# Optimization experiments

Hardware: AMD Instinct MI355X
Metric: run time of the kernel (lower is better)

Reference implementation:

```python
import jax, jax.numpy as jnp
import numpy as np
from jax import lax

B, N = 16, 2048
S0, S1, K = 256, 128, 32
EPS = 1e-5


def bn_relu(x, gamma, beta, axes):
    # training-mode BatchNorm (batch statistics) + ReLU; channel is last dim
    mean = jnp.mean(x, axis=axes, keepdims=True)
    var = jnp.var(x, axis=axes, keepdims=True)
    return jax.nn.relu((x - mean) * lax.rsqrt(var + EPS) * gamma + beta)


def fps(coords, s):
    # farthest point sampling, deterministic start at index 0. coords [B,N,3]
    b, n, _ = coords.shape
    def body(carry, _):
        dist, far = carry
        centroid = jnp.take_along_axis(coords, far[:, None, None], axis=1)  # [B,1,3]
        d = jnp.sum((coords - centroid) ** 2, axis=-1)                      # [B,N]
        dist = jnp.minimum(dist, d)
        return (dist, jnp.argmax(dist, axis=-1).astype(jnp.int32)), far
    init = (jnp.full((b, n), 1e10, coords.dtype), jnp.zeros((b,), jnp.int32))
    _, idx = lax.scan(body, init, None, length=s)
    return jnp.transpose(idx)  # [B,s]


def gather_points(pts, idx):
    # pts [B,N,C], idx [B,...] int -> [B,...,C]
    flat = idx.reshape(idx.shape[0], -1)[..., None]  # [B,M,1]
    out = jnp.take_along_axis(pts, flat, axis=1)     # [B,M,C]
    return out.reshape(*idx.shape, pts.shape[-1])


def sample_and_knn_group(s, k, coords, features):
    # coords [B,N,3], features [B,N,C] -> new_xyz [B,s,3], agg [B,s,k,2C]
    fps_idx = fps(coords, s)
    new_xyz = gather_points(coords, fps_idx)      # [B,s,3]
    center = gather_points(features, fps_idx)     # [B,s,C]
    d2 = jnp.sum((new_xyz[:, :, None, :] - coords[:, None, :, :]) ** 2, axis=-1)  # [B,s,N]
    _, knn_idx = lax.top_k(-d2, k)                # k smallest distances
    grouped = gather_points(features, knn_idx)    # [B,s,k,C]
    agg = jnp.concatenate(
        [grouped - center[:, :, None, :],
         jnp.broadcast_to(center[:, :, None, :], grouped.shape)], axis=-1)
    return new_xyz, agg


def sg_block(coords, features, s, k, w, gamma, beta):
    # conv1x1 -> BN -> ReLU -> max over k neighbors
    new_xyz, nf = sample_and_knn_group(s, k, coords, features)  # nf [B,s,k,d]
    h = jnp.einsum('bskd,od->bsko', nf, w)
    h = bn_relu(h, gamma, beta, axes=(0, 1, 2))
    return new_xyz, jnp.max(h, axis=2)  # [B,s,out]


def setup_inputs() -> dict:
    key = jax.random.key(0)
    ks = jax.random.split(key, 5)
    return {
        'x': jax.random.normal(ks[0], (B, 3, N), jnp.float32),
        'w1': jax.random.normal(ks[1], (64, 3), jnp.float32) * (1.0 / np.sqrt(3)),
        'g1': jnp.ones((64,), jnp.float32), 'b1': jnp.zeros((64,), jnp.float32),
        'w2': jax.random.normal(ks[2], (64, 64), jnp.float32) * 0.125,
        'g2': jnp.ones((64,), jnp.float32), 'b2': jnp.zeros((64,), jnp.float32),
        'w_sg0': jax.random.normal(ks[3], (128, 128), jnp.float32) * (1.0 / np.sqrt(128)),
        'g_sg0': jnp.ones((128,), jnp.float32), 'b_sg0': jnp.zeros((128,), jnp.float32),
        'w_sg1': jax.random.normal(ks[4], (256, 256), jnp.float32) * (1.0 / np.sqrt(256)),
        'g_sg1': jnp.ones((256,), jnp.float32), 'b_sg1': jnp.zeros((256,), jnp.float32),
    }


def reference(x, w1, g1, b1, w2, g2, b2, w_sg0, g_sg0, b_sg0, w_sg1, g_sg1, b_sg1):
    coords = jnp.transpose(x, (0, 2, 1))                   # [B,N,3]
    f = bn_relu(jnp.einsum('bnc,oc->bno', coords, w1), g1, b1, axes=(0, 1))  # [B,N,64]
    f = bn_relu(jnp.einsum('bnc,oc->bno', f, w2), g2, b2, axes=(0, 1))       # [B,N,64]
    xyz1, f1 = sg_block(coords, f, S0, K, w_sg0, g_sg0, b_sg0)   # [B,S0,128]
    _, f2 = sg_block(xyz1, f1, S1, K, w_sg1, g_sg1, b_sg1)       # [B,S1,256]
    return jnp.transpose(f2, (0, 2, 1))                           # [B,256,S1]
```

## Files before the change

### kernel.cpp

```cpp
#include <hip/hip_runtime.h>
#include <float.h>

#define BATCH 16
#define NPTS  2048
#define NS0   256
#define NS1   128
#define KK    32
#define EPSV  1e-5f
#define MROWS 32768.0f
#define M0F   131072.0f
#define M1F   65536.0f

__device__ __forceinline__ float sqdist(float ax,float ay,float az,float bx,float by,float bz){
  float dx=__fsub_rn(ax,bx), dy=__fsub_rn(ay,by), dz=__fsub_rn(az,bz);
  return __fadd_rn(__fadd_rn(__fmul_rn(dx,dx),__fmul_rn(dy,dy)),__fmul_rn(dz,dz));
}

template<int CTRL,int RM>
__device__ __forceinline__ float dpp_fmax_s(float x){
  int t = __builtin_amdgcn_update_dpp((int)0xFF800000, __float_as_int(x), CTRL, RM, 0xf, false);
  return fmaxf(x, __int_as_float(t));
}
template<int CTRL,int RM>
__device__ __forceinline__ unsigned dpp_umin_s(unsigned x){
  unsigned t = (unsigned)__builtin_amdgcn_update_dpp(-1, (int)x, CTRL, RM, 0xf, false);
  return t<x ? t : x;
}
__device__ __forceinline__ void wave_argmax_f32(float v, unsigned idx, float& mall, int& sel){
  float m=v;
  m=dpp_fmax_s<0x111,0xf>(m); m=dpp_fmax_s<0x112,0xf>(m); m=dpp_fmax_s<0x114,0xf>(m);
  m=dpp_fmax_s<0x118,0xf>(m); m=dpp_fmax_s<0x142,0xa>(m); m=dpp_fmax_s<0x143,0xc>(m);
  mall = __int_as_float(__builtin_amdgcn_readlane(__float_as_int(m),63));
  unsigned c = (v==mall)? idx : 0xFFFFFFFFu;
  c=dpp_umin_s<0x111,0xf>(c); c=dpp_umin_s<0x112,0xf>(c); c=dpp_umin_s<0x114,0xf>(c);
  c=dpp_umin_s<0x118,0xf>(c); c=dpp_umin_s<0x142,0xa>(c); c=dpp_umin_s<0x143,0xc>(c);
  sel = (int)(unsigned)__builtin_amdgcn_readlane((int)c,63);
}

template<int CTRL,int RM>
__device__ __forceinline__ unsigned long long dpp_umin64_s(unsigned long long x){
  unsigned tlo=(unsigned)__builtin_amdgcn_update_dpp(-1,(int)(unsigned)x,        CTRL,RM,0xf,false);
  unsigned thi=(unsigned)__builtin_amdgcn_update_dpp(-1,(int)(unsigned)(x>>32), CTRL,RM,0xf,false);
  unsigned long long t=((unsigned long long)thi<<32)|tlo;
  return t<x ? t : x;
}
__device__ __forceinline__ int wave_argmin_f32(float v, unsigned idx){
  unsigned long long k = ((unsigned long long)__float_as_uint(v)<<32) | (unsigned long long)idx;
  k=dpp_umin64_s<0x111,0xf>(k); k=dpp_umin64_s<0x112,0xf>(k); k=dpp_umin64_s<0x114,0xf>(k);
  k=dpp_umin64_s<0x118,0xf>(k); k=dpp_umin64_s<0x142,0xa>(k); k=dpp_umin64_s<0x143,0xc>(k);
  return (int)(unsigned)__builtin_amdgcn_readlane((int)(unsigned)k,63);
}


__device__ void embed1_body(int bid, const float* __restrict__ x, const float* __restrict__ w1,
                            float* __restrict__ coords, float* __restrict__ t1,
                            float* __restrict__ accS, float* __restrict__ accQ){
  __shared__ float w[192];
  __shared__ float xs[3][64];
  __shared__ float fin[64][65];
  __shared__ float ls[64], lq[64];
  int tid = threadIdx.x;
  if (tid < 192) w[tid] = w1[tid];
  int base = bid*64;
  int b = base / NPTS, n0 = base % NPTS;
  if (tid < 192){
    int ch = tid>>6, i = tid&63;
    xs[ch][i] = x[((size_t)b*3+ch)*NPTS + n0 + i];
  } else {
    int t = tid - 192;
    ls[t]=0.f; lq[t]=0.f;
  }
  __syncthreads();
  if (tid < 64){
    coords[(size_t)(base+tid)*3+0]=xs[0][tid];
    coords[(size_t)(base+tid)*3+1]=xs[1][tid];
    coords[(size_t)(base+tid)*3+2]=xs[2][tid];
  }
  int p = tid>>2, c0 = (tid&3)<<4;
  float cx=xs[0][p], cy=xs[1][p], cz=xs[2][p];
  #pragma unroll
  for(int j=0;j<16;j++){
    int c = c0+j;
    fin[p][c] = cx*w[c*3+0] + cy*w[c*3+1] + cz*w[c*3+2];
  }
  __syncthreads();
  float s_=0.f, q_=0.f;
  for(int i=tid;i<4096;i+=256){
    int pp=i>>6, c=i&63;
    float v = fin[pp][c];
    t1[(size_t)base*64 + i] = v;
    s_+=v; q_+=v*v;
  }
  atomicAdd(&ls[tid&63], s_);
  atomicAdd(&lq[tid&63], q_);
  __syncthreads();
  if(tid<64){ atomicAdd(accS+tid, ls[tid]); atomicAdd(accQ+tid, lq[tid]); }
}

__device__ void wt_body(int gid, const float* __restrict__ w0, float* __restrict__ wt0,
                        const float* __restrict__ w1, float* __restrict__ wt1){
  if(gid < 128*128){
    int o = gid % 128, c = gid / 128;
    wt0[gid] = w0[o*128 + c];
  } else {
    int g2 = gid - 128*128;
    if(g2 >= 256*256) return;
    int o = g2 % 256, c = g2 / 256;
    wt1[g2] = w1[o*256 + c];
  }
}

__device__ void embed2_body(int bid, const float* __restrict__ t1, const float* __restrict__ w2,
                            const float* __restrict__ accS, const float* __restrict__ accQ,
                            const float* __restrict__ g1, const float* __restrict__ b1,
                            float* __restrict__ t2,
                            float* __restrict__ acc2S, float* __restrict__ acc2Q,
                            float* ls, float* lq, char* smem){
  float (*fin)[64] = (float(*)[64])smem;
  float* sm = (float*)smem + 4096;
  float* sr = sm+64; float* sg = sr+64; float* sb = sg+64;
  int tid = threadIdx.x;
  if (tid<64){
    float S=accS[tid], Q=accQ[tid];
    float m = S/MROWS, v = Q/MROWS - m*m; if(v<0.f) v=0.f;
    sm[tid]=m; sr[tid]=rsqrtf(v+EPSV); sg[tid]=g1[tid]; sb[tid]=b1[tid];
    ls[tid]=0.f; lq[tid]=0.f;
  }
  __syncthreads();
  int base = bid*64;
  for(int i=tid;i<4096;i+=256){
    int p=i>>6, c=i&63;
    float v = t1[(size_t)(base+p)*64 + c];
    v = (v - sm[c])*sr[c]*sg[c] + sb[c];
    fin[p][c] = v>0.f ? v : 0.f;
  }
  __syncthreads();
  int o = tid & 63, p0 = tid>>6;
  float acc[16];
  #pragma unroll
  for(int i=0;i<16;i++) acc[i]=0.f;
  for(int cc=0; cc<64; cc+=4){
    float4 wv = *(const float4*)(w2 + o*64 + cc);
    #pragma unroll
    for(int i=0;i<16;i++){
      float4 f4 = *(const float4*)&fin[p0 + i*4][cc];
      acc[i] += f4.x*wv.x + f4.y*wv.y + f4.z*wv.z + f4.w*wv.w;
    }
  }
  float s=0.f,q=0.f;
  #pragma unroll
  for(int i=0;i<16;i++){
    float v = acc[i];
    t2[(size_t)(base+p0+i*4)*64 + o] = v;
    s+=v; q+=v*v;
  }
  atomicAdd(&ls[o], s);
  atomicAdd(&lq[o], q);
  __syncthreads();
  if(tid<64){ atomicAdd(acc2S+tid, ls[tid]); atomicAdd(acc2Q+tid, lq[tid]); }
}

template<int P, int S, int T>
__device__ void fps_body(int b, const float* __restrict__ x, int* __restrict__ outIdx,
                         float* __restrict__ outXyz, char* smem){
  constexpr int PPT = P/T;
  constexpr int NW  = T/64;
  float* sx=(float*)smem; float* sy=sx+P; float* sz=sy+P;
  int* sidx=(int*)(sz+P);
  unsigned long long* rv64=(unsigned long long*)(sidx+S);
  int tid = threadIdx.x;
  const float* xb = x + (size_t)b*3*P;
  float px[PPT], py[PPT], pz[PPT], dist[PPT];
  #pragma unroll
  for(int i=0;i<PPT;i++){
    int n = i*T + tid;
    float X=xb[n], Y=xb[P+n], Z=xb[2*P+n];
    px[i]=X; py[i]=Y; pz[i]=Z; dist[i]=1e10f;
    sx[n]=X; sy[n]=Y; sz[n]=Z;
  }
  __syncthreads();
  int cur = 0;
  float cx=sx[0], cy=sy[0], cz=sz[0];
  for(int s=0;s<S;s++){
    if(tid==0) sidx[s]=cur;
    if(s==S-1) break;
    float bv=-FLT_MAX; int bi=0;
    #pragma unroll
    for(int i=0;i<PPT;i++){
      float d = sqdist(px[i],py[i],pz[i],cx,cy,cz);
      float nd = fminf(dist[i], d);
      dist[i]=nd;
      int n = i*T + tid;
      if(nd>bv){ bv=nd; bi=n; }
    }
    float mall; int sel;
    wave_argmax_f32(bv,(unsigned)bi,mall,sel);
    int sl = s & 1;
    if((tid&63)==0) rv64[sl*NW+(tid>>6)] = ((unsigned long long)__float_as_uint(mall)<<32)|(unsigned)(~sel);
    __syncthreads();
    unsigned long long wk = rv64[sl*NW];
    #pragma unroll
    for(int w=1;w<NW;w++){ unsigned long long t = rv64[sl*NW+w]; if(t>wk) wk=t; }
    cur = (int)(~(unsigned)wk);
    cx=sx[cur]; cy=sy[cur]; cz=sz[cur];
  }
  __syncthreads();
  for(int i=tid; i<S; i+=T){
    int id = sidx[i];
    outIdx[b*S+i] = id;
    outXyz[((size_t)b*S+i)*3+0] = sx[id];
    outXyz[((size_t)b*S+i)*3+1] = sy[id];
    outXyz[((size_t)b*S+i)*3+2] = sz[id];
  }
}

template<int P, int S>
__device__ void fps_wave_body(int b, const float* __restrict__ pts, int* __restrict__ outIdx,
                              float* __restrict__ outXyz, char* smem){
  constexpr int PPT = P/64;
  float4* sp = (float4*)smem;
  int* sidx = (int*)(smem + P*sizeof(float4));
  int lane = threadIdx.x;
  const float* p = pts + (size_t)b*P*3;
  float px[PPT], py[PPT], pz[PPT], dist[PPT];
  #pragma unroll
  for(int i=0;i<PPT;i++){
    int n = i*64 + lane;
    float X=p[n*3], Y=p[n*3+1], Z=p[n*3+2];
    px[i]=X; py[i]=Y; pz[i]=Z; dist[i]=1e10f;
    sp[n] = make_float4(X,Y,Z,0.f);
  }
  __syncthreads();
  int cur = 0;
  float cx=sp[0].x, cy=sp[0].y, cz=sp[0].z;
  for(int s=0;s<S;s++){
    if(lane==0) sidx[s]=cur;
    if(s==S-1) break;
    float bv=-FLT_MAX; int bi=0;
    #pragma unroll
    for(int i=0;i<PPT;i++){
      float d = sqdist(px[i],py[i],pz[i],cx,cy,cz);
      float nd = fminf(dist[i], d);
      dist[i]=nd;
      int n = i*64 + lane;
      if(nd>bv){ bv=nd; bi=n; }
    }
    float mall; int sel;
    wave_argmax_f32(bv,(unsigned)bi,mall,sel);
    cur = sel;
    float4 cp = sp[cur];
    cx=cp.x; cy=cp.y; cz=cp.z;
  }
  __syncthreads();
  for(int i=lane; i<S; i+=64){
    int id = sidx[i];
    float4 cp = sp[id];
    outIdx[b*S+i] = id;
    outXyz[((size_t)b*S+i)*3+0] = cp.x;
    outXyz[((size_t)b*S+i)*3+1] = cp.y;
    outXyz[((size_t)b*S+i)*3+2] = cp.z;
  }
}

template<int P>
__device__ void knn_compute(const float* __restrict__ p, float qx, float qy, float qz,
                            int* outRow){
  constexpr int E = P/64;
  int lane = threadIdx.x & 63;
  float dl[E];
  float b1=FLT_MAX, b2=FLT_MAX;
  unsigned i1=0xFFFFFFFFu, i2=0xFFFFFFFFu, consumed=0u;
  #pragma unroll
  for(int i=0;i<E;i++){
    unsigned n = i*64 + lane;
    float v = sqdist(qx,qy,qz,p[n*3],p[n*3+1],p[n*3+2]);
    dl[i] = v;
    bool lt1 = v<b1, lt2 = v<b2;
    float    nb2 = lt1 ? b1 : (lt2 ? v : b2);
    unsigned ni2 = lt1 ? i1 : (lt2 ? n : i2);
    b1 = lt1 ? v : b1; i1 = lt1 ? n : i1;
    b2 = nb2; i2 = ni2;
  }
  for(int j=0;j<KK;j++){
    int sel = wave_argmin_f32(b1, i1);
    if(lane==0) outRow[j] = sel;
    if((sel & 63) == lane){
      consumed |= 1u << (sel >> 6);
      b1 = b2; i1 = i2;
      b2 = FLT_MAX; i2 = 0xFFFFFFFFu;
      if(b1 == FLT_MAX){
        #pragma unroll
        for(int i=0;i<E;i++){
          float v = ((consumed>>i)&1u) ? FLT_MAX : dl[i];
          unsigned n = i*64 + lane;
          bool lt1 = v<b1, lt2 = v<b2;
          float    nb2 = lt1 ? b1 : (lt2 ? v : b2);
          unsigned ni2 = lt1 ? i1 : (lt2 ? n : i2);
          b1 = lt1 ? v : b1; i1 = lt1 ? n : i1;
          b2 = nb2; i2 = ni2;
        }
      }
    }
  }
}

template<int C, int P, int MODE>
__device__ void pass1_body(int bq, const float* __restrict__ feats, const float* __restrict__ feats2,
                           const int* knnrow, int ci, const float* __restrict__ WT,
                           float* __restrict__ hmax, float* __restrict__ hmin,
                           float* __restrict__ part, int S,
                           const float* __restrict__ accS, const float* __restrict__ accQ,
                           const float* __restrict__ bg, const float* __restrict__ bb,
                           char* smem){
  constexpr int O   = 2*C;
  constexpr int TPB = C;
  constexpr int C4  = C/4;
  constexpr int OG  = O/8;
  constexpr int LDC = C+4;
  float* gfp = (float*)smem;
  float* cf  = gfp + KK*LDC;
  float* sa  = cf + C;
  float* sbb = sa + C;
  float* sct = sbb + C;
  int tid = threadIdx.x;
  int b = bq / S;
  const float* fb = feats + (size_t)b*P*C;
  const float* fb2 = (MODE==2) ? feats2 + (size_t)b*P*C : nullptr;
  {
    float Mv = (MODE==1) ? MROWS : M0F;
    float S_=accS[tid], Q_=accQ[tid];
    float m = S_/Mv, vv = Q_/Mv - m*m; if(vv<0.f) vv=0.f;
    float a = rsqrtf(vv+EPSV)*bg[tid];
    float sh = bb[tid] - m*a;
    sa[tid]=a; sbb[tid]=sh;
    float raw;
    if(MODE==1) raw = fb[(size_t)ci*C + tid];
    else        raw = (a>=0.f) ? fb[(size_t)ci*C + tid] : fb2[(size_t)ci*C + tid];
    float cv = a*raw + sh;
    cf[tid] = cv>0.f ? cv : 0.f;
  }
  __syncthreads();
  for(int i=tid; i<KK*C4; i+=TPB){
    int k = i/C4, d4 = i - k*C4;
    size_t row = (size_t)knnrow[k]*C;
    float4 a4 = *(const float4*)&sa[d4*4];
    float4 s4 = *(const float4*)&sbb[d4*4];
    float4 c4 = *(const float4*)&cf[d4*4];
    float4 g  = ((const float4*)(fb + row))[d4];
    float4 r;
    if(MODE==2){
      float4 g2 = ((const float4*)(fb2 + row))[d4];
      float gx = (a4.x>=0.f? g.x : g2.x)*a4.x + s4.x; gx = gx>0.f?gx:0.f;
      float gy = (a4.y>=0.f? g.y : g2.y)*a4.y + s4.y; gy = gy>0.f?gy:0.f;
      float gz = (a4.z>=0.f? g.z : g2.z)*a4.z + s4.z; gz = gz>0.f?gz:0.f;
      float gw = (a4.w>=0.f? g.w : g2.w)*a4.w + s4.w; gw = gw>0.f?gw:0.f;
      r.x=gx-c4.x; r.y=gy-c4.y; r.z=gz-c4.z; r.w=gw-c4.w;
    } else {
      float gx = a4.x*g.x+s4.x; gx = gx>0.f?gx:0.f;
      float gy = a4.y*g.y+s4.y; gy = gy>0.f?gy:0.f;
      float gz = a4.z*g.z+s4.z; gz = gz>0.f?gz:0.f;
      float gw = a4.w*g.w+s4.w; gw = gw>0.f?gw:0.f;
      r.x=gx-c4.x; r.y=gy-c4.y; r.z=gz-c4.z; r.w=gw-c4.w;
    }
    *(float4*)&gfp[k*LDC + d4*4] = r;
  }
  __syncthreads();
  {
    int o2 = tid*2;
    float ct0=0.f, ct1=0.f;
    for(int c=0;c<C;c+=4){
      float4 c4 = *(const float4*)&cf[c];
      #pragma unroll
      for(int t=0;t<4;t++){
        float cv = ((const float*)&c4)[t];
        float2 wh = *(const float2*)&WT[(size_t)(C+c+t)*O + o2];
        ct0 += cv*wh.x; ct1 += cv*wh.y;
      }
    }
    sct[o2]=ct0; sct[o2+1]=ct1;
  }
  __syncthreads();
  int kg = tid / OG;
  int og = tid % OG;
  float acc[8][8];
  #pragma unroll
  for(int a=0;a<8;a++)
    #pragma unroll
    for(int bb2=0;bb2<8;bb2++) acc[a][bb2]=0.f;
  for(int dc=0; dc<C4; dc++){
    float4 g4[8];
    #pragma unroll
    for(int jk=0;jk<8;jk++) g4[jk] = *(const float4*)&gfp[(kg*8+jk)*LDC + dc*4];
    #pragma unroll
    for(int t=0;t<4;t++){
      const float* wrow = WT + (size_t)(dc*4+t)*O + og*8;
      float4 wa = *(const float4*)wrow;
      float4 wb = *(const float4*)(wrow+4);
      #pragma unroll
      for(int jk=0;jk<8;jk++){
        float gs = ((const float*)&g4[jk])[t];
        acc[jk][0] += gs*wa.x; acc[jk][1] += gs*wa.y; acc[jk][2] += gs*wa.z; acc[jk][3] += gs*wa.w;
        acc[jk][4] += gs*wb.x; acc[jk][5] += gs*wb.y; acc[jk][6] += gs*wb.z; acc[jk][7] += gs*wb.w;
      }
    }
  }
  float tmx[8],tmn[8],tsm[8],tsq[8];
  #pragma unroll
  for(int jo=0;jo<8;jo++){
    int o = og*8+jo;
    float ct = sct[o];
    float s=0.f,q=0.f,mx=-FLT_MAX,mn=FLT_MAX;
    #pragma unroll
    for(int jk=0;jk<8;jk++){
      float h = acc[jk][jo] + ct;
      s+=h; q+=h*h; mx=fmaxf(mx,h); mn=fminf(mn,h);
    }
    tmx[jo]=mx; tmn[jo]=mn; tsm[jo]=s; tsq[jo]=q;
  }
  if constexpr (TPB==64){
    #pragma unroll
    for(int jo=0;jo<8;jo++){
      tmx[jo]=fmaxf(tmx[jo],__shfl_xor(tmx[jo],16)); tmx[jo]=fmaxf(tmx[jo],__shfl_xor(tmx[jo],32));
      tmn[jo]=fminf(tmn[jo],__shfl_xor(tmn[jo],16)); tmn[jo]=fminf(tmn[jo],__shfl_xor(tmn[jo],32));
      tsm[jo]+=__shfl_xor(tsm[jo],16); tsm[jo]+=__shfl_xor(tsm[jo],32);
      tsq[jo]+=__shfl_xor(tsq[jo],16); tsq[jo]+=__shfl_xor(tsq[jo],32);
    }
    if(tid<OG){
      #pragma unroll
      for(int jo=0;jo<8;jo++){
        int o = tid*8+jo;
        hmax[(size_t)bq*O+o]=tmx[jo]; hmin[(size_t)bq*O+o]=tmn[jo];
        part[(size_t)bq*2*O+o]=tsm[jo]; part[(size_t)bq*2*O+O+o]=tsq[jo];
      }
    }
  } else {
    #pragma unroll
    for(int jo=0;jo<8;jo++){
      tmx[jo]=fmaxf(tmx[jo],__shfl_xor(tmx[jo],32));
      tmn[jo]=fminf(tmn[jo],__shfl_xor(tmn[jo],32));
      tsm[jo]+=__shfl_xor(tsm[jo],32);
      tsq[jo]+=__shfl_xor(tsq[jo],32);
    }
    int wv = tid>>6;
    if((tid&63)<32){
      int og_ = tid&31;
      size_t rb = (size_t)bq*2 + wv;
      #pragma unroll
      for(int jo=0;jo<8;jo++){
        int o = og_*8+jo;
        hmax[rb*O+o]=tmx[jo]; hmin[rb*O+o]=tmn[jo];
        part[rb*2*O+o]=tsm[jo]; part[rb*2*O+O+o]=tsq[jo];
      }
    }
  }
}


__global__ __launch_bounds__(256) void k_embed1_wt(const float* __restrict__ x, const float* __restrict__ w1,
                         float* __restrict__ coords, float* __restrict__ t1,
                         const float* __restrict__ wsg0, float* __restrict__ wt0,
                         const float* __restrict__ wsg1, float* __restrict__ wt1,
                         float* __restrict__ acc1S, float* __restrict__ acc1Q){
  if(blockIdx.x < 512) embed1_body(blockIdx.x, x, w1, coords, t1, acc1S, acc1Q);
  else wt_body((blockIdx.x-512)*256 + threadIdx.x, wsg0, wt0, wsg1, wt1);
}

__global__ __launch_bounds__(256, 1) void k_fps0_embed2(const float* __restrict__ x,
                         int* __restrict__ fps0, float* __restrict__ xyz0,
                         const float* __restrict__ t1, const float* __restrict__ w2,
                         const float* __restrict__ acc1S, const float* __restrict__ acc1Q,
                         const float* __restrict__ g1, const float* __restrict__ b1,
                         float* __restrict__ t2,
                         float* __restrict__ acc2S, float* __restrict__ acc2Q){
  extern __shared__ char smem[];
  __shared__ float ls[64], lq[64];
  if(blockIdx.x < BATCH) fps_body<NPTS,NS0,256>(blockIdx.x, x, fps0, xyz0, smem);
  else embed2_body(blockIdx.x-BATCH, t1, w2, acc1S, acc1Q, g1, b1, t2, acc2S, acc2Q, ls, lq, smem);
}

__global__ __launch_bounds__(64, 2) void k_fps1_p1a(const float* __restrict__ xyz0,
                         int* __restrict__ fps1, float* __restrict__ xyz1,
                         const float* __restrict__ coords, const float* __restrict__ t2,
                         const int* __restrict__ fps0, const float* __restrict__ wt0,
                         float* __restrict__ hmax0, float* __restrict__ hmin0, float* __restrict__ part0,
                         const float* __restrict__ acc2S, const float* __restrict__ acc2Q,
                         const float* __restrict__ g2, const float* __restrict__ b2){
  __shared__ __align__(16) char SU[10112];
  if(blockIdx.x < BATCH){
    fps_wave_body<NS0,NS1>(blockIdx.x, xyz0, fps1, xyz1, SU);
    return;
  }
  int bq = blockIdx.x - BATCH;
  int b = bq / NS0;
  int* sknn = (int*)(SU + 9984);
  const float* pc = coords + (size_t)b*NPTS*3;
  float qx=xyz0[(size_t)bq*3], qy=xyz0[(size_t)bq*3+1], qz=xyz0[(size_t)bq*3+2];
  knn_compute<NPTS>(pc, qx, qy, qz, sknn);
  __syncthreads();
  pass1_body<64,NPTS,1>(bq, t2, nullptr, sknn, fps0[bq], wt0, hmax0, hmin0, part0, NS0,
                        acc2S, acc2Q, g2, b2, SU);
}

__global__ __launch_bounds__(256) void k_statsB(const float* __restrict__ part, int W,
                                                float* __restrict__ acc){
  int tid = threadIdx.x;
  int r0 = blockIdx.x*64;
  for(int c=tid; c<W; c+=256){
    float a=0.f;
    for(int r=0;r<64;r++) a += part[(size_t)(r0+r)*W + c];
    atomicAdd(acc+c, a);
  }
}

__global__ __launch_bounds__(128, 2) void k_knn1_p1b(const float* __restrict__ xyz0,
                         const float* __restrict__ xyz1, const int* __restrict__ fps1,
                         const float* __restrict__ hmax0, const float* __restrict__ hmin0,
                         const float* __restrict__ wt1,
                         float* __restrict__ hmax1, float* __restrict__ hmin1, float* __restrict__ part1,
                         const float* __restrict__ accB0S, const float* __restrict__ accB0Q,
                         const float* __restrict__ gsg0, const float* __restrict__ bsg0){
  __shared__ __align__(16) char SU[19584];
  int bq = blockIdx.x;
  int b = bq / NS1;
  int* sknn = (int*)(SU + 19456);
  if(threadIdx.x < 64){
    const float* pts = xyz0 + (size_t)b*NS0*3;
    float qx=xyz1[(size_t)bq*3], qy=xyz1[(size_t)bq*3+1], qz=xyz1[(size_t)bq*3+2];
    knn_compute<NS0>(pts, qx, qy, qz, sknn);
  }
  __syncthreads();
  pass1_body<128,NS0,2>(bq, hmax0, hmin0, sknn, fps1[bq], wt1, hmax1, hmin1, part1, NS1,
                        accB0S, accB0Q, gsg0, bsg0, SU);
}

__global__ __launch_bounds__(256) void k_post1tr(const float* __restrict__ hmax, const float* __restrict__ hmin,
        const float* __restrict__ aS, const float* __restrict__ aQ,
        const float* __restrict__ g, const float* __restrict__ bb, float* __restrict__ out){
  __shared__ float ssc[64], ssh[64];
  __shared__ float tile[64][129];
  int tid = threadIdx.x;
  int blk = blockIdx.x; int b = blk>>2; int c0 = (blk&3)*64;
  if(tid<64){
    int o = c0+tid;
    float m = aS[o]/M1F, v = aQ[o]/M1F - m*m; if(v<0.f) v=0.f;
    float sc = rsqrtf(v+EPSV)*g[o];
    ssc[tid]=sc; ssh[tid]=bb[o]-m*sc;
  }
  __syncthreads();
  for(int i=tid; i<128*64; i+=256){
    int r=i>>6, ch=i&63;
    size_t rb = (size_t)(b*NS1+r)*2;
    float sc = ssc[ch];
    float va = hmax[rb*256 + c0+ch], vb = hmax[(rb+1)*256 + c0+ch];
    float wa = hmin[rb*256 + c0+ch], wb = hmin[(rb+1)*256 + c0+ch];
    float h = (sc>=0.f) ? fmaxf(va,vb) : fminf(wa,wb);
    float v = h*sc + ssh[ch];
    tile[ch][r] = v>0.f ? v : 0.f;
  }
  __syncthreads();
  for(int i=tid; i<64*128; i+=256){
    int ch=i>>7, s=i&127;
    out[(size_t)b*(256*NS1) + (size_t)(c0+ch)*NS1 + s] = tile[ch][s];
  }
}

extern "C" void kernel_launch(void* const* d_in, const int* in_sizes, int n_in,
                              void* d_out, int out_size, void* d_ws, size_t ws_size,
                              hipStream_t stream){
  const float* x    = (const float*)d_in[0];
  const float* w1   = (const float*)d_in[1];
  const float* g1   = (const float*)d_in[2];
  const float* b1   = (const float*)d_in[3];
  const float* w2   = (const float*)d_in[4];
  const float* g2   = (const float*)d_in[5];
  const float* b2   = (const float*)d_in[6];
  const float* wsg0 = (const float*)d_in[7];
  const float* gsg0 = (const float*)d_in[8];
  const float* bsg0 = (const float*)d_in[9];
  const float* wsg1 = (const float*)d_in[10];
  const float* gsg1 = (const float*)d_in[11];
  const float* bsg1 = (const float*)d_in[12];
  float* out = (float*)d_out;

  float* wsf = (float*)d_ws;
  float* coords = wsf;                    wsf += BATCH*NPTS*3;
  float* t1     = wsf;                    wsf += BATCH*NPTS*64;
  float* t2     = wsf;                    wsf += BATCH*NPTS*64;
  float* acc1S=wsf; wsf+=64;  float* acc1Q=wsf; wsf+=64;
  float* acc2S=wsf; wsf+=64;  float* acc2Q=wsf; wsf+=64;
  float* accB0=wsf; wsf+=256;
  float* accB1=wsf; wsf+=512;
  int*   fps0 = (int*)wsf;                wsf += BATCH*NS0;
  float* xyz0 = wsf;                      wsf += BATCH*NS0*3;
  float* hmax0= wsf;                      wsf += BATCH*NS0*128;
  float* hmin0= wsf;                      wsf += BATCH*NS0*128;
  float* part0= wsf;                      wsf += BATCH*NS0*2*128;
  int*   fps1 = (int*)wsf;                wsf += BATCH*NS1;
  float* xyz1 = wsf;                      wsf += BATCH*NS1*3;
  float* wt0  = wsf;                      wsf += 128*128;
  float* wt1  = wsf;                      wsf += 256*256;
  float* part1 = t1;
  float* hmax1 = t2;
  float* hmin1 = t2 + BATCH*NS1*2*256;

  const int DYN_L3 = (NPTS*3 + NS0)*4 + 2*4*8;

  hipMemsetAsync(acc1S, 0, 1024*sizeof(float), stream);
  k_embed1_wt<<<dim3(832), dim3(256), 0, stream>>>(x, w1, coords, t1, wsg0, wt0, wsg1, wt1,
                                                   acc1S, acc1Q);
  k_fps0_embed2<<<dim3(BATCH+512), dim3(256), DYN_L3, stream>>>(x, fps0, xyz0,
                                                  t1, w2, acc1S, acc1Q, g1, b1, t2, acc2S, acc2Q);
  k_fps1_p1a<<<dim3(BATCH + BATCH*NS0), dim3(64), 0, stream>>>(xyz0, fps1, xyz1,
                                                  coords, t2, fps0, wt0,
                                                  hmax0, hmin0, part0,
                                                  acc2S, acc2Q, g2, b2);
  k_statsB<<<dim3(64), dim3(256), 0, stream>>>(part0, 256, accB0);
  k_knn1_p1b<<<dim3(BATCH*NS1), dim3(128), 0, stream>>>(xyz0, xyz1, fps1,
                                                  hmax0, hmin0, wt1,
                                                  hmax1, hmin1, part1,
                                                  accB0, accB0+128, gsg0, bsg0);
  k_statsB<<<dim3(64), dim3(256), 0, stream>>>(part1, 512, accB1);
  k_post1tr<<<dim3(64), dim3(256), 0, stream>>>(hmax1, hmin1, accB1, accB1+256, gsg1, bsg1, out);
}
```

Measured before the change: 394.2 us.

## Stream FPS0 progress into persistent mega-kernel overlapping KNN/pass1a and FPS1

Splits FPS0 out of the embed2 kernel and merges FPS0, FPS1 and the first KNN+conv pass into one persistent kernel that takes work tickets from an atomic counter. FPS0 publishes its sampled indices and coordinates incrementally, raising a per-batch progress flag every 32 samples. KNN/pass1a waves spin-wait on that flag, so neighbour search for early centroids can start while FPS is still running. The change also packs four single-wave work items into each 256-thread block. It adds spin-wait and memory-ordering risk and depends on ticket order to avoid deadlock.

```diff
diff --git a/kernel.cpp b/kernel.cpp
--- a/kernel.cpp
+++ b/kernel.cpp
@@ -49,6 +49,19 @@
   k=dpp_umin64_s<0x111,0xf>(k); k=dpp_umin64_s<0x112,0xf>(k); k=dpp_umin64_s<0x114,0xf>(k);
   k=dpp_umin64_s<0x118,0xf>(k); k=dpp_umin64_s<0x142,0xa>(k); k=dpp_umin64_s<0x143,0xc>(k);
   return (int)(unsigned)__builtin_amdgcn_readlane((int)(unsigned)k,63);
+}
+
+__device__ __forceinline__ void wave_sync(){
+  asm volatile("s_waitcnt lgkmcnt(0)" ::: "memory");
+  __builtin_amdgcn_sched_barrier(0);
+}
+
+__device__ __forceinline__ void wait_ge(int* flag, int want){
+  for(int t=0; t<(1<<20); ++t){
+    if(__hip_atomic_load(flag, __ATOMIC_RELAXED, __HIP_MEMORY_SCOPE_AGENT) >= want) break;
+    __builtin_amdgcn_s_sleep(2);
+  }
+  asm volatile("" ::: "memory");
 }
 
 
@@ -162,7 +175,7 @@
 
 template<int P, int S, int T>
 __device__ void fps_body(int b, const float* __restrict__ x, int* __restrict__ outIdx,
-                         float* __restrict__ outXyz, char* smem){
+                         float* __restrict__ outXyz, char* smem, int* prog){
   constexpr int PPT = P/T;
   constexpr int NW  = T/64;
   float* sx=(float*)smem; float* sy=sx+P; float* sz=sy+P;
@@ -182,7 +195,14 @@
   int cur = 0;
   float cx=sx[0], cy=sy[0], cz=sz[0];
   for(int s=0;s<S;s++){
-    if(tid==0) sidx[s]=cur;
+    if(tid==0){
+      sidx[s]=cur;
+      size_t o = (size_t)b*S + s;
+      outIdx[o]=cur;
+      outXyz[o*3+0]=cx; outXyz[o*3+1]=cy; outXyz[o*3+2]=cz;
+      if((s&31)==31)
+        __hip_atomic_store(prog+b, s+1, __ATOMIC_RELEASE, __HIP_MEMORY_SCOPE_AGENT);
+    }
     if(s==S-1) break;
     float bv=-FLT_MAX; int bi=0;
     #pragma unroll
@@ -212,25 +232,30 @@
     outXyz[((size_t)b*S+i)*3+1] = sy[id];
     outXyz[((size_t)b*S+i)*3+2] = sz[id];
   }
+  __syncthreads();
+  if(tid==0)
+    __hip_atomic_store(prog+b, S, __ATOMIC_RELEASE, __HIP_MEMORY_SCOPE_AGENT);
 }
 
 template<int P, int S>
-__device__ void fps_wave_body(int b, const float* __restrict__ pts, int* __restrict__ outIdx,
-                              float* __restrict__ outXyz, char* smem){
+__device__ void fps1_wave(int b, float* __restrict__ pts, int* __restrict__ outIdx,
+                          float* __restrict__ outXyz, char* smem){
   constexpr int PPT = P/64;
   float4* sp = (float4*)smem;
   int* sidx = (int*)(smem + P*sizeof(float4));
-  int lane = threadIdx.x;
-  const float* p = pts + (size_t)b*P*3;
+  int lane = threadIdx.x & 63;
+  float* p = pts + (size_t)b*P*3;
   float px[PPT], py[PPT], pz[PPT], dist[PPT];
   #pragma unroll
   for(int i=0;i<PPT;i++){
     int n = i*64 + lane;
-    float X=p[n*3], Y=p[n*3+1], Z=p[n*3+2];
+    float X=__hip_atomic_load(p+n*3+0, __ATOMIC_RELAXED, __HIP_MEMORY_SCOPE_AGENT);
+    float Y=__hip_atomic_load(p+n*3+1, __ATOMIC_RELAXED, __HIP_MEMORY_SCOPE_AGENT);
+    float Z=__hip_atomic_load(p+n*3+2, __ATOMIC_RELAXED, __HIP_MEMORY_SCOPE_AGENT);
     px[i]=X; py[i]=Y; pz[i]=Z; dist[i]=1e10f;
     sp[n] = make_float4(X,Y,Z,0.f);
   }
-  __syncthreads();
+  wave_sync();
   int cur = 0;
   float cx=sp[0].x, cy=sp[0].y, cz=sp[0].z;
   for(int s=0;s<S;s++){
@@ -251,7 +276,7 @@
     float4 cp = sp[cur];
     cx=cp.x; cy=cp.y; cz=cp.z;
   }
-  __syncthreads();
+  wave_sync();
   for(int i=lane; i<S; i+=64){
     int id = sidx[i];
     float4 cp = sp[id];
@@ -300,6 +325,117 @@
           b2 = nb2; i2 = ni2;
         }
       }
+    }
+  }
+}
+
+__device__ void pass1a_wave(int bq, const float* __restrict__ feats,
+                            const int* knnrow, int ci, const float* __restrict__ WT,
+                            float* __restrict__ hmax, float* __restrict__ hmin,
+                            float* __restrict__ part,
+                            const float* __restrict__ accS, const float* __restrict__ accQ,
+                            const float* __restrict__ bg, const float* __restrict__ bb,
+                            char* smem){
+  constexpr int C=64, O=128, C4=16, OG=16, LDC=68;
+  float* gfp = (float*)smem;
+  float* cf  = gfp + KK*LDC;
+  float* sa  = cf + C;
+  float* sbb = sa + C;
+  float* sct = sbb + C;
+  int lane = threadIdx.x & 63;
+  int b = bq >> 8;
+  const float* fb = feats + (size_t)b*NPTS*C;
+  {
+    float S_=accS[lane], Q_=accQ[lane];
+    float m = S_/MROWS, vv = Q_/MROWS - m*m; if(vv<0.f) vv=0.f;
+    float a = rsqrtf(vv+EPSV)*bg[lane];
+    float sh = bb[lane] - m*a;
+    sa[lane]=a; sbb[lane]=sh;
+    float raw = fb[(size_t)ci*C + lane];
+    float cv = a*raw + sh;
+    cf[lane] = cv>0.f ? cv : 0.f;
+  }
+  wave_sync();
+  for(int i=lane; i<KK*C4; i+=64){
+    int k = i>>4, d4 = i&15;
+    size_t row = (size_t)knnrow[k]*C;
+    float4 a4 = *(const float4*)&sa[d4*4];
+    float4 s4 = *(const float4*)&sbb[d4*4];
+    float4 c4 = *(const float4*)&cf[d4*4];
+    float4 g  = ((const float4*)(fb + row))[d4];
+    float gx = a4.x*g.x+s4.x; gx = gx>0.f?gx:0.f;
+    float gy = a4.y*g.y+s4.y; gy = gy>0.f?gy:0.f;
+    float gz = a4.z*g.z+s4.z; gz = gz>0.f?gz:0.f;
+    float gw = a4.w*g.w+s4.w; gw = gw>0.f?gw:0.f;
+    float4 r; r.x=gx-c4.x; r.y=gy-c4.y; r.z=gz-c4.z; r.w=gw-c4.w;
+    *(float4*)&gfp[k*LDC + d4*4] = r;
+  }
+  wave_sync();
+  {
+    int o2 = lane*2;
+    float ct0=0.f, ct1=0.f;
+    for(int c=0;c<C;c+=4){
+      float4 c4 = *(const float4*)&cf[c];
+      #pragma unroll
+      for(int t=0;t<4;t++){
+        float cv = ((const float*)&c4)[t];
+        float2 wh = *(const float2*)&WT[(size_t)(C+c+t)*O + o2];
+        ct0 += cv*wh.x; ct1 += cv*wh.y;
+      }
+    }
+    sct[o2]=ct0; sct[o2+1]=ct1;
+  }
+  wave_sync();
+  int kg = lane >> 4;
+  int og = lane & 15;
+  float acc[8][8];
+  #pragma unroll
+  for(int a=0;a<8;a++)
+    #pragma unroll
+    for(int bb2=0;bb2<8;bb2++) acc[a][bb2]=0.f;
+  for(int dc=0; dc<C4; dc++){
+    float4 g4[8];
+    #pragma unroll
+    for(int jk=0;jk<8;jk++) g4[jk] = *(const float4*)&gfp[(kg*8+jk)*LDC + dc*4];
+    #pragma unroll
+    for(int t=0;t<4;t++){
+      const float* wrow = WT + (size_t)(dc*4+t)*O + og*8;
+      float4 wa = *(const float4*)wrow;
+      float4 wb = *(const float4*)(wrow+4);
+      #pragma unroll
+      for(int jk=0;jk<8;jk++){
+        float gs = ((const float*)&g4[jk])[t];
+        acc[jk][0] += gs*wa.x; acc[jk][1] += gs*wa.y; acc[jk][2] += gs*wa.z; acc[jk][3] += gs*wa.w;
+        acc[jk][4] += gs*wb.x; acc[jk][5] += gs*wb.y; acc[jk][6] += gs*wb.z; acc[jk][7] += gs*wb.w;
+      }
+    }
+  }
+  float tmx[8],tmn[8],tsm[8],tsq[8];
+  #pragma unroll
+  for(int jo=0;jo<8;jo++){
+    int o = og*8+jo;
+    float ct = sct[o];
+    float s=0.f,q=0.f,mx=-FLT_MAX,mn=FLT_MAX;
+    #pragma unroll
+    for(int jk=0;jk<8;jk++){
+      float h = acc[jk][jo] + ct;
+      s+=h; q+=h*h; mx=fmaxf(mx,h); mn=fminf(mn,h);
+    }
+    tmx[jo]=mx; tmn[jo]=mn; tsm[jo]=s; tsq[jo]=q;
+  }
+  #pragma unroll
+  for(int jo=0;jo<8;jo++){
+    tmx[jo]=fmaxf(tmx[jo],__shfl_xor(tmx[jo],16)); tmx[jo]=fmaxf(tmx[jo],__shfl_xor(tmx[jo],32));
+    tmn[jo]=fminf(tmn[jo],__shfl_xor(tmn[jo],16)); tmn[jo]=fminf(tmn[jo],__shfl_xor(tmn[jo],32));
+    tsm[jo]+=__shfl_xor(tsm[jo],16); tsm[jo]+=__shfl_xor(tsm[jo],32);
+    tsq[jo]+=__shfl_xor(tsq[jo],16); tsq[jo]+=__shfl_xor(tsq[jo],32);
+  }
+  if(lane<OG){
+    #pragma unroll
+    for(int jo=0;jo<8;jo++){
+      int o = lane*8+jo;
+      hmax[(size_t)bq*O+o]=tmx[jo]; hmin[(size_t)bq*O+o]=tmn[jo];
+      part[(size_t)bq*2*O+o]=tsm[jo]; part[(size_t)bq*2*O+O+o]=tsq[jo];
     }
   }
 }
@@ -417,40 +553,22 @@
     }
     tmx[jo]=mx; tmn[jo]=mn; tsm[jo]=s; tsq[jo]=q;
   }
-  if constexpr (TPB==64){
+  #pragma unroll
+  for(int jo=0;jo<8;jo++){
+    tmx[jo]=fmaxf(tmx[jo],__shfl_xor(tmx[jo],32));
+    tmn[jo]=fminf(tmn[jo],__shfl_xor(tmn[jo],32));
+    tsm[jo]+=__shfl_xor(tsm[jo],32);
+    tsq[jo]+=__shfl_xor(tsq[jo],32);
+  }
+  int wv = tid>>6;
+  if((tid&63)<32){
+    int og_ = tid&31;
+    size_t rb = (size_t)bq*2 + wv;
     #pragma unroll
     for(int jo=0;jo<8;jo++){
-      tmx[jo]=fmaxf(tmx[jo],__shfl_xor(tmx[jo],16)); tmx[jo]=fmaxf(tmx[jo],__shfl_xor(tmx[jo],32));
-      tmn[jo]=fminf(tmn[jo],__shfl_xor(tmn[jo],16)); tmn[jo]=fminf(tmn[jo],__shfl_xor(tmn[jo],32));
-      tsm[jo]+=__shfl_xor(tsm[jo],16); tsm[jo]+=__shfl_xor(tsm[jo],32);
-      tsq[jo]+=__shfl_xor(tsq[jo],16); tsq[jo]+=__shfl_xor(tsq[jo],32);
-    }
-    if(tid<OG){
-      #pragma unroll
-      for(int jo=0;jo<8;jo++){
-        int o = tid*8+jo;
-        hmax[(size_t)bq*O+o]=tmx[jo]; hmin[(size_t)bq*O+o]=tmn[jo];
-        part[(size_t)bq*2*O+o]=tsm[jo]; part[(size_t)bq*2*O+O+o]=tsq[jo];
-      }
-    }
-  } else {
-    #pragma unroll
-    for(int jo=0;jo<8;jo++){
-      tmx[jo]=fmaxf(tmx[jo],__shfl_xor(tmx[jo],32));
-      tmn[jo]=fminf(tmn[jo],__shfl_xor(tmn[jo],32));
-      tsm[jo]+=__shfl_xor(tsm[jo],32);
-      tsq[jo]+=__shfl_xor(tsq[jo],32);
-    }
-    int wv = tid>>6;
-    if((tid&63)<32){
-      int og_ = tid&31;
-      size_t rb = (size_t)bq*2 + wv;
-      #pragma unroll
-      for(int jo=0;jo<8;jo++){
-        int o = og_*8+jo;
-        hmax[rb*O+o]=tmx[jo]; hmin[rb*O+o]=tmn[jo];
-        part[rb*2*O+o]=tsm[jo]; part[rb*2*O+O+o]=tsq[jo];
-      }
+      int o = og_*8+jo;
+      hmax[rb*O+o]=tmx[jo]; hmin[rb*O+o]=tmn[jo];
+      part[rb*2*O+o]=tsm[jo]; part[rb*2*O+O+o]=tsq[jo];
     }
   }
 }
@@ -465,40 +583,62 @@
   else wt_body((blockIdx.x-512)*256 + threadIdx.x, wsg0, wt0, wsg1, wt1);
 }
 
-__global__ __launch_bounds__(256, 1) void k_fps0_embed2(const float* __restrict__ x,
-                         int* __restrict__ fps0, float* __restrict__ xyz0,
-                         const float* __restrict__ t1, const float* __restrict__ w2,
+__global__ __launch_bounds__(256, 1) void k_embed2(const float* __restrict__ t1, const float* __restrict__ w2,
                          const float* __restrict__ acc1S, const float* __restrict__ acc1Q,
                          const float* __restrict__ g1, const float* __restrict__ b1,
                          float* __restrict__ t2,
                          float* __restrict__ acc2S, float* __restrict__ acc2Q){
   extern __shared__ char smem[];
   __shared__ float ls[64], lq[64];
-  if(blockIdx.x < BATCH) fps_body<NPTS,NS0,256>(blockIdx.x, x, fps0, xyz0, smem);
-  else embed2_body(blockIdx.x-BATCH, t1, w2, acc1S, acc1Q, g1, b1, t2, acc2S, acc2Q, ls, lq, smem);
-}
-
-__global__ __launch_bounds__(64, 2) void k_fps1_p1a(const float* __restrict__ xyz0,
-                         int* __restrict__ fps1, float* __restrict__ xyz1,
-                         const float* __restrict__ coords, const float* __restrict__ t2,
-                         const int* __restrict__ fps0, const float* __restrict__ wt0,
+  embed2_body(blockIdx.x, t1, w2, acc1S, acc1Q, g1, b1, t2, acc2S, acc2Q, ls, lq, smem);
+}
+
+#define NT_FPS0  16
+#define NT_FPS1E 20
+#define NT_ALL   1044
+__global__ __launch_bounds__(256) void k_mega(const float* __restrict__ x,
+                         int* __restrict__ fps0i, float* __restrict__ xyz0,
+                         const float* __restrict__ t2,
+                         const float* __restrict__ acc2S, const float* __restrict__ acc2Q,
+                         const float* __restrict__ coords, const float* __restrict__ wt0,
                          float* __restrict__ hmax0, float* __restrict__ hmin0, float* __restrict__ part0,
-                         const float* __restrict__ acc2S, const float* __restrict__ acc2Q,
-                         const float* __restrict__ g2, const float* __restrict__ b2){
-  __shared__ __align__(16) char SU[10112];
-  if(blockIdx.x < BATCH){
-    fps_wave_body<NS0,NS1>(blockIdx.x, xyz0, fps1, xyz1, SU);
-    return;
-  }
-  int bq = blockIdx.x - BATCH;
-  int b = bq / NS0;
-  int* sknn = (int*)(SU + 9984);
-  const float* pc = coords + (size_t)b*NPTS*3;
-  float qx=xyz0[(size_t)bq*3], qy=xyz0[(size_t)bq*3+1], qz=xyz0[(size_t)bq*3+2];
-  knn_compute<NPTS>(pc, qx, qy, qz, sknn);
-  __syncthreads();
-  pass1_body<64,NPTS,1>(bq, t2, nullptr, sknn, fps0[bq], wt0, hmax0, hmin0, part0, NS0,
-                        acc2S, acc2Q, g2, b2, SU);
+                         const float* __restrict__ g2, const float* __restrict__ b2,
+                         int* __restrict__ fps1i, float* __restrict__ xyz1,
+                         int* prog, int* tck){
+  extern __shared__ __align__(16) char SU[];
+  __shared__ int sTk;
+  int tid = threadIdx.x;
+  for(;;){
+    if(tid==0) sTk = atomicAdd(tck, 1);
+    __syncthreads();
+    int tk = sTk;
+    __syncthreads();
+    if(tk >= NT_ALL) return;
+    if(tk < NT_FPS0){
+      fps_body<NPTS,NS0,256>(tk, x, fps0i, xyz0, SU, prog);
+    } else if(tk < NT_FPS1E){
+      int wv = tid>>6;
+      int b4 = (tk-NT_FPS0)*4 + wv;
+      wait_ge(prog + b4, NS0);
+      fps1_wave<NS0,NS1>(b4, xyz0, fps1i, xyz1, SU + wv*4608);
+    } else {
+      int q = tk - NT_FPS1E;
+      int wv = tid>>6;
+      int b = q & 15;
+      int s = ((q>>4)<<2) + wv;
+      int bq = (b<<8) + s;
+      char* W = SU + wv*10112;
+      int* sknn = (int*)(W + 9984);
+      wait_ge(prog + b, s + 1);
+      float qx = __hip_atomic_load(xyz0+(size_t)bq*3+0, __ATOMIC_RELAXED, __HIP_MEMORY_SCOPE_AGENT);
+      float qy = __hip_atomic_load(xyz0+(size_t)bq*3+1, __ATOMIC_RELAXED, __HIP_MEMORY_SCOPE_AGENT);
+      float qz = __hip_atomic_load(xyz0+(size_t)bq*3+2, __ATOMIC_RELAXED, __HIP_MEMORY_SCOPE_AGENT);
+      int   ci = __hip_atomic_load(fps0i+bq, __ATOMIC_RELAXED, __HIP_MEMORY_SCOPE_AGENT);
+      knn_compute<NPTS>(coords + (size_t)b*NPTS*3, qx, qy, qz, sknn);
+      wave_sync();
+      pass1a_wave(bq, t2, sknn, ci, wt0, hmax0, hmin0, part0, acc2S, acc2Q, g2, b2, W);
+    }
+  }
 }
 
 __global__ __launch_bounds__(256) void k_statsB(const float* __restrict__ part, int W,
@@ -590,6 +730,9 @@
   float* acc2S=wsf; wsf+=64;  float* acc2Q=wsf; wsf+=64;
   float* accB0=wsf; wsf+=256;
   float* accB1=wsf; wsf+=512;
+  int*   prog = (int*)wsf;                wsf += 16;
+  int*   tck  = (int*)wsf;                wsf += 1;
+  wsf += 15;
   int*   fps0 = (int*)wsf;                wsf += BATCH*NS0;
   float* xyz0 = wsf;                      wsf += BATCH*NS0*3;
   float* hmax0= wsf;                      wsf += BATCH*NS0*128;
@@ -603,17 +746,18 @@
   float* hmax1 = t2;
   float* hmin1 = t2 + BATCH*NS1*2*256;
 
-  const int DYN_L3 = (NPTS*3 + NS0)*4 + 2*4*8;
-
-  hipMemsetAsync(acc1S, 0, 1024*sizeof(float), stream);
+  const int DYN_E2   = (4096 + 256)*4;
+  const int DYN_MEGA = 4*10112;
+
+  hipMemsetAsync(acc1S, 0, (1024+32)*sizeof(float), stream);
   k_embed1_wt<<<dim3(832), dim3(256), 0, stream>>>(x, w1, coords, t1, wsg0, wt0, wsg1, wt1,
                                                    acc1S, acc1Q);
-  k_fps0_embed2<<<dim3(BATCH+512), dim3(256), DYN_L3, stream>>>(x, fps0, xyz0,
-                                                  t1, w2, acc1S, acc1Q, g1, b1, t2, acc2S, acc2Q);
-  k_fps1_p1a<<<dim3(BATCH + BATCH*NS0), dim3(64), 0, stream>>>(xyz0, fps1, xyz1,
-                                                  coords, t2, fps0, wt0,
-                                                  hmax0, hmin0, part0,
-                                                  acc2S, acc2Q, g2, b2);
+  k_embed2<<<dim3(512), dim3(256), DYN_E2, stream>>>(t1, w2, acc1S, acc1Q, g1, b1,
+                                                     t2, acc2S, acc2Q);
+  k_mega<<<dim3(NT_ALL), dim3(256), DYN_MEGA, stream>>>(x, fps0, xyz0,
+                                                  t2, acc2S, acc2Q,
+                                                  coords, wt0, hmax0, hmin0, part0, g2, b2,
+                                                  fps1, xyz1, prog, tck);
   k_statsB<<<dim3(64), dim3(256), 0, stream>>>(part0, 256, accB0);
   k_knn1_p1b<<<dim3(BATCH*NS1), dim3(128), 0, stream>>>(xyz0, xyz1, fps1,
                                                   hmax0, hmin0, wt1,
```

New measurement: 442.0 us. 12.1% more time.
